# Optimization experiments

Hardware: AMD Instinct MI355X
Metric: run time of the kernel (lower is better)

## Reference

```python
import jax, jax.numpy as jnp
import numpy as np

D = 256; NH = 8; DH = D // NH; NL = 4; NP = 4; DFFN = 1024
SPATIAL = [(128, 128), (64, 64), (32, 32), (16, 16)]
LEN_IN = sum(h * w for h, w in SPATIAL)
N, LQ = 8, 1000


def _ln(x, g, b, eps=1e-5):
    m = jnp.mean(x, -1, keepdims=True)
    v = jnp.mean((x - m) ** 2, -1, keepdims=True)
    return (x - m) * jax.lax.rsqrt(v + eps) * g + b


def _ms_deform_core(value, loc, attn_w):
    # value (N,Len_in,NH,DH); loc (N,Lq,NH,NL,NP,2) in [0,1]; attn_w (N,Lq,NH,NL,NP)
    n, lq = loc.shape[0], loc.shape[1]
    out = jnp.zeros((n, NH, lq, DH), value.dtype)
    start = 0
    for l, (Hl, Wl) in enumerate(SPATIAL):
        v = value[:, start:start + Hl * Wl].transpose(0, 2, 1, 3)  # (N,NH,HW,DH)
        start += Hl * Wl
        # grid_sample-style mapping, align_corners=False, zero padding
        x = loc[:, :, :, l, :, 0] * Wl - 0.5  # (N,Lq,NH,NP)
        y = loc[:, :, :, l, :, 1] * Hl - 0.5
        x0 = jnp.floor(x); y0 = jnp.floor(y)
        lx = x - x0; ly = y - y0
        x0i = x0.astype(jnp.int32); y0i = y0.astype(jnp.int32)
        acc = jnp.zeros((n, NH, lq, NP, DH), value.dtype)
        for dy, dx, w in ((0, 0, (1 - ly) * (1 - lx)), (0, 1, (1 - ly) * lx),
                          (1, 0, ly * (1 - lx)), (1, 1, ly * lx)):
            xi = x0i + dx; yi = y0i + dy
            valid = ((xi >= 0) & (xi < Wl) & (yi >= 0) & (yi < Hl)).astype(value.dtype)
            idx = jnp.clip(yi, 0, Hl - 1) * Wl + jnp.clip(xi, 0, Wl - 1)  # (N,Lq,NH,NP)
            idx = idx.transpose(0, 2, 1, 3).reshape(n, NH, lq * NP)
            g = jnp.take_along_axis(v, idx[..., None], axis=2).reshape(n, NH, lq, NP, DH)
            acc = acc + g * (w * valid).transpose(0, 2, 1, 3)[..., None]
        out = out + jnp.sum(acc * attn_w[:, :, :, l].transpose(0, 2, 1, 3)[..., None], axis=3)
    return out.transpose(0, 2, 1, 3).reshape(n, lq, D)


def setup_inputs() -> dict:
    key = jax.random.key(0)
    ks = jax.random.split(key, 16)
    s = 0.02
    inp = {
        'tgt': jax.random.normal(ks[0], (N, LQ, D), jnp.float32),
        'query_pos': jax.random.normal(ks[1], (N, LQ, D), jnp.float32),
        'reference_points': jax.random.uniform(ks[2], (N, LQ, NL, 2), jnp.float32),
        'src': jax.random.normal(ks[3], (N, LEN_IN, D), jnp.float32),
        'spatial_shapes': jnp.array(SPATIAL, jnp.int32),
        'level_start_index': jnp.array(np.cumsum([0] + [h * w for h, w in SPATIAL[:-1]]), jnp.int32),
        # self-attention
        'sa_in_w': jax.random.normal(ks[4], (3 * D, D), jnp.float32) * s,
        'sa_in_b': jnp.zeros((3 * D,), jnp.float32),
        'sa_out_w': jax.random.normal(ks[5], (D, D), jnp.float32) * s,
        'sa_out_b': jnp.zeros((D,), jnp.float32),
        'norm2_g': jnp.ones((D,), jnp.float32), 'norm2_b': jnp.zeros((D,), jnp.float32),
        # MSDeformAttn
        'off_w': jax.random.normal(ks[6], (NH * NL * NP * 2, D), jnp.float32) * s,
        'off_b': jax.random.normal(ks[7], (NH * NL * NP * 2,), jnp.float32) * s,
        'aw_w': jax.random.normal(ks[8], (NH * NL * NP, D), jnp.float32) * s,
        'aw_b': jnp.zeros((NH * NL * NP,), jnp.float32),
        'val_w': jax.random.normal(ks[9], (D, D), jnp.float32) * s,
        'val_b': jnp.zeros((D,), jnp.float32),
        'outp_w': jax.random.normal(ks[10], (D, D), jnp.float32) * s,
        'outp_b': jnp.zeros((D,), jnp.float32),
        'norm1_g': jnp.ones((D,), jnp.float32), 'norm1_b': jnp.zeros((D,), jnp.float32),
        # FFN
        'ffn_w1': jax.random.normal(ks[11], (DFFN, D), jnp.float32) * s,
        'ffn_b1': jnp.zeros((DFFN,), jnp.float32),
        'ffn_w2': jax.random.normal(ks[12], (D, DFFN), jnp.float32) * s,
        'ffn_b2': jnp.zeros((D,), jnp.float32),
        'norm3_g': jnp.ones((D,), jnp.float32), 'norm3_b': jnp.zeros((D,), jnp.float32),
    }
    return inp


def reference(tgt, query_pos, reference_points, src, spatial_shapes, level_start_index,
              sa_in_w, sa_in_b, sa_out_w, sa_out_b, norm2_g, norm2_b,
              off_w, off_b, aw_w, aw_b, val_w, val_b, outp_w, outp_b, norm1_g, norm1_b,
              ffn_w1, ffn_b1, ffn_w2, ffn_b2, norm3_g, norm3_b):
    n, lq, _ = tgt.shape
    # ---- self-attention (q = k = tgt + pos, v = tgt), eval mode (dropout off)
    qk = tgt + query_pos
    wq, wk, wv = sa_in_w[:D], sa_in_w[D:2 * D], sa_in_w[2 * D:]
    bq, bk, bv = sa_in_b[:D], sa_in_b[D:2 * D], sa_in_b[2 * D:]
    q = (qk @ wq.T + bq).reshape(n, lq, NH, DH)
    k = (qk @ wk.T + bk).reshape(n, lq, NH, DH)
    v = (tgt @ wv.T + bv).reshape(n, lq, NH, DH)
    scores = jnp.einsum('bqhd,bkhd->bhqk', q, k) / np.sqrt(DH).astype(np.float32)
    attn = jax.nn.softmax(scores, axis=-1)
    sa = jnp.einsum('bhqk,bkhd->bqhd', attn, v).reshape(n, lq, D) @ sa_out_w.T + sa_out_b
    tgt = _ln(tgt + sa, norm2_g, norm2_b)
    # ---- multi-scale deformable cross-attention
    query = tgt + query_pos
    value = (src @ val_w.T + val_b).reshape(n, LEN_IN, NH, DH)
    offsets = (query @ off_w.T + off_b).reshape(n, lq, NH, NL, NP, 2)
    aw = (query @ aw_w.T + aw_b).reshape(n, lq, NH, NL * NP)
    aw = jax.nn.softmax(aw, axis=-1).reshape(n, lq, NH, NL, NP)
    # offset normalizer: (W_l, H_l)
    norm = jnp.stack([spatial_shapes[:, 1], spatial_shapes[:, 0]], -1).astype(tgt.dtype)
    loc = reference_points[:, :, None, :, None, :] + offsets / norm[None, None, None, :, None, :]
    ca = _ms_deform_core(value, loc, aw) @ outp_w.T + outp_b
    tgt = _ln(tgt + ca, norm1_g, norm1_b)
    # ---- FFN
    ff = jax.nn.relu(tgt @ ffn_w1.T + ffn_b1) @ ffn_w2.T + ffn_b2
    tgt = _ln(tgt + ff, norm3_g, norm3_b)
    return tgt
```

## Files before the change

### kernel.cpp

```cpp
#include <hip/hip_runtime.h>
#include <hip/hip_bf16.h>

#define D 256
#define NH 8
#define DH 32
#define NL 4
#define NP 4
#define DFFN 1024
#define LEN_IN 21760
#define NB 8
#define LQ 1000

typedef __hip_bfloat16 bf16;
typedef __attribute__((ext_vector_type(8))) short s8v;
typedef __attribute__((ext_vector_type(4))) float f4v;

template <typename T> __device__ inline T fromF(float x);
template <> __device__ inline float fromF<float>(float x) { return x; }
template <> __device__ inline bf16 fromF<bf16>(float x) { return __float2bfloat16(x); }

__device__ inline short bfr(float f) {
    unsigned u = __float_as_uint(f);
    u += 0x7fff + ((u >> 16) & 1);
    return (short)(u >> 16);
}
__device__ inline s8v pack8(float4 x, float4 y) {
    s8v r;
    r[0] = bfr(x.x); r[1] = bfr(x.y); r[2] = bfr(x.z); r[3] = bfr(x.w);
    r[4] = bfr(y.x); r[5] = bfr(y.y); r[6] = bfr(y.z); r[7] = bfr(y.w);
    return r;
}

__device__ inline unsigned cvtpk(float a, float b) {
    unsigned r;
    asm("v_cvt_pk_bf16_f32 %0, %1, %2" : "=v"(r) : "v"(a), "v"(b));
    return r;
}
__device__ inline s8v pkcvt8(float4 a, float4 b) {
    union { s8v v; unsigned u[4]; } r;
    r.u[0] = cvtpk(a.x, a.y);
    r.u[1] = cvtpk(a.z, a.w);
    r.u[2] = cvtpk(b.x, b.y);
    r.u[3] = cvtpk(b.z, b.w);
    return r.v;
}

__device__ __forceinline__ void gload_lds16(const void* gsrc, void* ldst) {
    __builtin_amdgcn_global_load_lds(
        (const __attribute__((address_space(1))) unsigned int*)gsrc,
        (__attribute__((address_space(3))) unsigned int*)ldst,
        16, 0, 0);
}

__global__ __launch_bounds__(256) void pack_weights(const float* __restrict__ s0, const float* __restrict__ s1,
                                                    const float* __restrict__ s2, const float* __restrict__ s3,
                                                    const float* __restrict__ s4, const float* __restrict__ s5,
                                                    const float* __restrict__ s6, const float* __restrict__ s7,
                                                    bf16* __restrict__ dst) {
    int g = blockIdx.x * 256 + threadIdx.x;
    const float* s; int base;
    if      (g <  49152) { s = s0; base = 0;      }
    else if (g <  65536) { s = s1; base = 49152;  }
    else if (g <  81920) { s = s2; base = 65536;  }
    else if (g <  90112) { s = s3; base = 81920;  }
    else if (g < 106496) { s = s4; base = 90112;  }
    else if (g < 122880) { s = s5; base = 106496; }
    else if (g < 188416) { s = s6; base = 122880; }
    else                 { s = s7; base = 188416; }
    float4 v = ((const float4*)s)[g - base];
    short4 o; o.x = bfr(v.x); o.y = bfr(v.y); o.z = bfr(v.z); o.w = bfr(v.w);
    ((short4*)dst)[g] = o;
}

template <typename TA, typename TC, int MT, bool ADD2, int KK>
__global__ __launch_bounds__(256) void gemm_direct(const TA* __restrict__ A, const float* __restrict__ A2,
                                                   const bf16* __restrict__ W, const float* __restrict__ bias,
                                                   TC* __restrict__ C, int N, int do_relu) {
    const int tid = threadIdx.x;
    const int lane = tid & 63, wave = tid >> 6;
    const int fr = lane & 15, fq = lane >> 4;
    const int n0 = blockIdx.x * 128;
    const int wrow = blockIdx.y * (MT * 32) + (wave >> 1) * (MT * 16);
    const int wn = n0 + (wave & 1) * 64;

    const TA* ap[MT];
    const float* a2p[MT];
#pragma unroll
    for (int i = 0; i < MT; ++i) {
        size_t r = (size_t)(wrow + i * 16 + fr);
        ap[i] = A + r * KK + fq * 8;
        if constexpr (ADD2) a2p[i] = A2 + r * KK + fq * 8;
    }
    const bf16* wp[4];
#pragma unroll
    for (int j = 0; j < 4; ++j) wp[j] = W + (size_t)(wn + j * 16 + fr) * KK + fq * 8;

    f4v acc[MT][4];
#pragma unroll
    for (int i = 0; i < MT; ++i)
#pragma unroll
        for (int j = 0; j < 4; ++j) acc[i][j] = (f4v){0.f, 0.f, 0.f, 0.f};

    auto step = [&](int k0) {
        s8v bfv[4];
#pragma unroll
        for (int j = 0; j < 4; ++j) bfv[j] = *(const s8v*)(wp[j] + k0);
        s8v af[MT];
#pragma unroll
        for (int i = 0; i < MT; ++i) {
            if constexpr (sizeof(TA) == 2) {
                af[i] = *(const s8v*)((const bf16*)ap[i] + k0);
            } else {
                float4 x0 = *(const float4*)((const float*)ap[i] + k0);
                float4 x1 = *(const float4*)((const float*)ap[i] + k0 + 4);
                if constexpr (ADD2) {
                    float4 y0 = *(const float4*)(a2p[i] + k0);
                    float4 y1 = *(const float4*)(a2p[i] + k0 + 4);
                    x0.x += y0.x; x0.y += y0.y; x0.z += y0.z; x0.w += y0.w;
                    x1.x += y1.x; x1.y += y1.y; x1.z += y1.z; x1.w += y1.w;
                }
                af[i] = pkcvt8(x0, x1);
            }
        }
#pragma unroll
        for (int i = 0; i < MT; ++i)
#pragma unroll
            for (int j = 0; j < 4; ++j)
                acc[i][j] = __builtin_amdgcn_mfma_f32_16x16x32_bf16(af[i], bfv[j], acc[i][j], 0, 0, 0);
    };

    if constexpr (KK <= 256) {
#pragma unroll
        for (int k0 = 0; k0 < KK; k0 += 32) step(k0);
    } else {
#pragma unroll 4
        for (int k0 = 0; k0 < KK; k0 += 32) step(k0);
    }

#pragma unroll
    for (int j = 0; j < 4; ++j) {
        const int col = wn + j * 16 + fr;
        const float bb = bias[col];
#pragma unroll
        for (int i = 0; i < MT; ++i) {
            const int rbase = wrow + i * 16 + fq * 4;
#pragma unroll
            for (int r = 0; r < 4; ++r) {
                float v = acc[i][j][r] + bb;
                if (do_relu) v = fmaxf(v, 0.f);
                C[(size_t)(rbase + r) * N + col] = fromF<TC>(v);
            }
        }
    }
}

__global__ __launch_bounds__(256) void gemm_val(const float* __restrict__ A, const bf16* __restrict__ W,
                                                const float* __restrict__ bias, bf16* __restrict__ C) {
    __shared__ float As[4096];
    const int tid = threadIdx.x;
    const int lane = tid & 63, wave = tid >> 6;
    const int fr = lane & 15, fq = lane >> 4;
    const int m0 = blockIdx.y * 128;
    const int wm = (wave >> 1) * 64;
    const int wn = blockIdx.x * 128 + (wave & 1) * 64;

    int srow[4], soff[4];
#pragma unroll
    for (int g = 0; g < 4; ++g) {
        int s = g * 4096 + tid * 16;
        int r = s >> 7;
        srow[g] = r;
        soff[g] = (s & 127) ^ ((r & 7) << 4);
    }
    int rb[4][2];
#pragma unroll
    for (int i = 0; i < 4; ++i) {
        int r2 = wm + i * 16 + fr;
        rb[i][0] = r2 * 128 + ((fq * 32) ^ ((r2 & 7) << 4));
        rb[i][1] = r2 * 128 + ((fq * 32 + 16) ^ ((r2 & 7) << 4));
    }
    const bf16* wp[4];
#pragma unroll
    for (int j = 0; j < 4; ++j) wp[j] = W + (size_t)(wn + j * 16 + fr) * 256 + fq * 8;

    f4v acc[4][4];
#pragma unroll
    for (int i = 0; i < 4; ++i)
#pragma unroll
        for (int j = 0; j < 4; ++j) acc[i][j] = (f4v){0.f, 0.f, 0.f, 0.f};

#pragma unroll
    for (int kk = 0; kk < 8; ++kk) {
        const int k0 = kk * 32;
        __syncthreads();
#pragma unroll
        for (int g = 0; g < 4; ++g) {
            const char* gsrc = (const char*)(A + (size_t)(m0 + srow[g]) * 256 + k0) + soff[g];
            gload_lds16(gsrc, (char*)As + g * 4096 + tid * 16);
        }
        __syncthreads();
        s8v bfv[4];
#pragma unroll
        for (int j = 0; j < 4; ++j) bfv[j] = *(const s8v*)(wp[j] + k0);
        s8v af[4];
#pragma unroll
        for (int i = 0; i < 4; ++i) {
            float4 x0 = *(const float4*)((const char*)As + rb[i][0]);
            float4 x1 = *(const float4*)((const char*)As + rb[i][1]);
            af[i] = pkcvt8(x0, x1);
        }
#pragma unroll
        for (int i = 0; i < 4; ++i)
#pragma unroll
            for (int j = 0; j < 4; ++j)
                acc[i][j] = __builtin_amdgcn_mfma_f32_16x16x32_bf16(af[i], bfv[j], acc[i][j], 0, 0, 0);
    }

#pragma unroll
    for (int j = 0; j < 4; ++j) {
        const int col = wn + j * 16 + fr;
        const float bb = bias[col];
#pragma unroll
        for (int i = 0; i < 4; ++i) {
            const int rbase = m0 + wm + i * 16 + fq * 4;
#pragma unroll
            for (int r = 0; r < 4; ++r) {
                float v = acc[i][j][r] + bb;
                C[(size_t)(rbase + r) * 256 + col] = fromF<bf16>(v);
            }
        }
    }
}

__global__ __launch_bounds__(256) void attn_mfma(const float* __restrict__ q, const float* __restrict__ k,
                                                 const float* __restrict__ v, float* __restrict__ out) {
    const int h = blockIdx.y, n = blockIdx.z;
    const int tid = threadIdx.x, wave = tid >> 6, lane = tid & 63;
    const int fr = lane & 15, fq = lane >> 4;
    __shared__ short Ks[32 * 40];
    __shared__ short Vt[32 * 40];
    __shared__ short Pl[4][16 * 40];
    const int q0 = blockIdx.x * 64 + wave * 16;

    s8v qfrag;
    {
        int qr = q0 + fr; if (qr >= LQ) qr = LQ - 1;
        const float* qp = q + ((size_t)(n * LQ + qr)) * D + h * DH + fq * 8;
        float4 t0 = *(const float4*)qp;
        float4 t1 = *(const float4*)(qp + 4);
        const float sc = 0.17677669529663687f;
        t0.x *= sc; t0.y *= sc; t0.z *= sc; t0.w *= sc;
        t1.x *= sc; t1.y *= sc; t1.z *= sc; t1.w *= sc;
        qfrag = pack8(t0, t1);
    }

    f4v O0 = {0.f, 0.f, 0.f, 0.f}, O1 = {0.f, 0.f, 0.f, 0.f};
    float mrow[4] = {-1e30f, -1e30f, -1e30f, -1e30f};
    float lrow[4] = {0.f, 0.f, 0.f, 0.f};

    for (int kt = 0; kt < LQ; kt += 32) {
        __syncthreads();
        {
            int key = tid >> 3, d4 = (tid & 7) * 4;
            int gk = kt + key; if (gk >= LQ) gk = LQ - 1;
            const float* kp = k + ((size_t)(n * LQ + gk)) * D + h * DH + d4;
            float4 t = *(const float4*)kp;
            short4 pk; pk.x = bfr(t.x); pk.y = bfr(t.y); pk.z = bfr(t.z); pk.w = bfr(t.w);
            *(short4*)&Ks[key * 40 + d4] = pk;
        }
        {
            int d = tid & 31, key0 = (tid >> 5) * 4;
            float vv[4];
#pragma unroll
            for (int i = 0; i < 4; ++i) {
                int gk = kt + key0 + i; if (gk >= LQ) gk = LQ - 1;
                vv[i] = v[((size_t)(n * LQ + gk)) * D + h * DH + d];
            }
            short4 pk; pk.x = bfr(vv[0]); pk.y = bfr(vv[1]); pk.z = bfr(vv[2]); pk.w = bfr(vv[3]);
            *(short4*)&Vt[d * 40 + key0] = pk;
        }
        __syncthreads();

        f4v s0 = {0.f, 0.f, 0.f, 0.f}, s1 = {0.f, 0.f, 0.f, 0.f};
        s8v kf0 = *(s8v*)&Ks[fr * 40 + fq * 8];
        s8v kf1 = *(s8v*)&Ks[(16 + fr) * 40 + fq * 8];
        s0 = __builtin_amdgcn_mfma_f32_16x16x32_bf16(qfrag, kf0, s0, 0, 0, 0);
        s1 = __builtin_amdgcn_mfma_f32_16x16x32_bf16(qfrag, kf1, s1, 0, 0, 0);
        const bool val0 = (kt + fr) < LQ, val1 = (kt + 16 + fr) < LQ;

        float p0[4], p1[4], alpha[4];
#pragma unroll
        for (int r = 0; r < 4; ++r) {
            float a = val0 ? s0[r] : -1e30f;
            float b = val1 ? s1[r] : -1e30f;
            float mx = fmaxf(a, b);
            mx = fmaxf(mx, __shfl_xor(mx, 1, 64));
            mx = fmaxf(mx, __shfl_xor(mx, 2, 64));
            mx = fmaxf(mx, __shfl_xor(mx, 4, 64));
            mx = fmaxf(mx, __shfl_xor(mx, 8, 64));
            float mnew = fmaxf(mrow[r], mx);
            float al = __expf(mrow[r] - mnew);
            float e0 = __expf(a - mnew);
            float e1 = __expf(b - mnew);
            float ps = e0 + e1;
            ps += __shfl_xor(ps, 1, 64);
            ps += __shfl_xor(ps, 2, 64);
            ps += __shfl_xor(ps, 4, 64);
            ps += __shfl_xor(ps, 8, 64);
            lrow[r] = lrow[r] * al + ps;
            mrow[r] = mnew;
            alpha[r] = al;
            p0[r] = e0; p1[r] = e1;
        }

        short* pw = Pl[wave];
#pragma unroll
        for (int r = 0; r < 4; ++r) {
            pw[(fq * 4 + r) * 40 + fr] = bfr(p0[r]);
            pw[(fq * 4 + r) * 40 + 16 + fr] = bfr(p1[r]);
        }
        __builtin_amdgcn_s_waitcnt(0);
        s8v pfrag = *(s8v*)&pw[fr * 40 + fq * 8];
        s8v vf0 = *(s8v*)&Vt[fr * 40 + fq * 8];
        s8v vf1 = *(s8v*)&Vt[(16 + fr) * 40 + fq * 8];
#pragma unroll
        for (int r = 0; r < 4; ++r) { O0[r] *= alpha[r]; O1[r] *= alpha[r]; }
        O0 = __builtin_amdgcn_mfma_f32_16x16x32_bf16(pfrag, vf0, O0, 0, 0, 0);
        O1 = __builtin_amdgcn_mfma_f32_16x16x32_bf16(pfrag, vf1, O1, 0, 0, 0);
    }

#pragma unroll
    for (int r = 0; r < 4; ++r) {
        int qrow = q0 + fq * 4 + r;
        if (qrow < LQ) {
            float inv = 1.0f / lrow[r];
            float* op = out + ((size_t)(n * LQ + qrow)) * D + h * DH;
            op[fr] = O0[r] * inv;
            op[16 + fr] = O1[r] * inv;
        }
    }
}

__global__ __launch_bounds__(256) void ln_res_kernel(const float* __restrict__ base, const float* __restrict__ delta,
                                                     const float* __restrict__ g, const float* __restrict__ b,
                                                     float* __restrict__ out) {
    __shared__ float scratch[8];
    const size_t row = blockIdx.x;
    const int d = threadIdx.x;
    float x = base[row * D + d] + delta[row * D + d];
    float s1 = x, s2 = x * x;
    for (int o = 32; o > 0; o >>= 1) {
        s1 += __shfl_down(s1, o, 64);
        s2 += __shfl_down(s2, o, 64);
    }
    const int w = threadIdx.x >> 6, lane = threadIdx.x & 63;
    if (lane == 0) { scratch[w] = s1; scratch[4 + w] = s2; }
    __syncthreads();
    s1 = scratch[0] + scratch[1] + scratch[2] + scratch[3];
    s2 = scratch[4] + scratch[5] + scratch[6] + scratch[7];
    float mean = s1 * (1.0f / 256.0f);
    float var = s2 * (1.0f / 256.0f) - mean * mean;
    float rstd = rsqrtf(var + 1e-5f);
    float y = (x - mean) * rstd * g[d] + b[d];
    out[row * D + d] = y;
}

__global__ __launch_bounds__(256) void aw_softmax_kernel(float* __restrict__ aw, int ngrp) {
    int t = blockIdx.x * 256 + threadIdx.x;
    if (t >= ngrp) return;
    float* p = aw + (size_t)t * 16;
    float m = p[0];
#pragma unroll
    for (int i = 1; i < 16; ++i) m = fmaxf(m, p[i]);
    float s = 0.f;
    float e[16];
#pragma unroll
    for (int i = 0; i < 16; ++i) { e[i] = __expf(p[i] - m); s += e[i]; }
    float inv = 1.0f / s;
#pragma unroll
    for (int i = 0; i < 16; ++i) p[i] = e[i] * inv;
}

__global__ __launch_bounds__(256) void deform_kernel(const bf16* __restrict__ value, const float* __restrict__ offs,
                                                     const float* __restrict__ aw, const float* __restrict__ refp,
                                                     float* __restrict__ out) {
    const int h = blockIdx.y, n = blockIdx.z;
    const int tid = threadIdx.x;
    const int wave = tid >> 6, lane = tid & 63;
    const int qi = blockIdx.x * 4 + wave;
    const int c = lane & 15;
    const int l = lane >> 4;
    const size_t row = (size_t)n * LQ + qi;
    const int W = 128 >> l, H = 128 >> l;
    const int START[4] = {0, 16384, 20480, 21504};
    const float invW = 1.0f / W, invH = 1.0f / H;

    const float rx = refp[(row * NL + l) * 2 + 0];
    const float ry = refp[(row * NL + l) * 2 + 1];
    const bf16* vbase = value + ((size_t)n * LEN_IN + START[l]) * D + h * DH + 2 * c;
    const float* offp = offs + row * D + (h * NL + l) * NP * 2;
    const float* awp = aw + row * 128 + h * 16 + l * 4;

    float acc0 = 0.f, acc1 = 0.f;
#pragma unroll
    for (int p = 0; p < 4; ++p) {
        float ox = offp[p * 2 + 0];
        float oy = offp[p * 2 + 1];
        float wa = awp[p];
        float x = (rx + ox * invW) * W - 0.5f;
        float y = (ry + oy * invH) * H - 0.5f;
        float xf = floorf(x), yf = floorf(y);
        float lx = x - xf, ly = y - yf;
        int x0 = (int)xf, y0 = (int)yf;
        int x1 = x0 + 1, y1 = y0 + 1;
        float vx0 = (x0 >= 0 && x0 < W) ? 1.f : 0.f;
        float vx1 = (x1 >= 0 && x1 < W) ? 1.f : 0.f;
        float vy0 = (y0 >= 0 && y0 < H) ? 1.f : 0.f;
        float vy1 = (y1 >= 0 && y1 < H) ? 1.f : 0.f;
        int x0c = min(max(x0, 0), W - 1), x1c = min(max(x1, 0), W - 1);
        int y0c = min(max(y0, 0), H - 1), y1c = min(max(y1, 0), H - 1);
        float w00 = wa * (1.f - ly) * (1.f - lx) * vy0 * vx0;
        float w01 = wa * (1.f - ly) * lx * vy0 * vx1;
        float w10 = wa * ly * (1.f - lx) * vy1 * vx0;
        float w11 = wa * ly * lx * vy1 * vx1;
        unsigned u00 = *(const unsigned*)(vbase + (size_t)(y0c * W + x0c) * D);
        unsigned u01 = *(const unsigned*)(vbase + (size_t)(y0c * W + x1c) * D);
        unsigned u10 = *(const unsigned*)(vbase + (size_t)(y1c * W + x0c) * D);
        unsigned u11 = *(const unsigned*)(vbase + (size_t)(y1c * W + x1c) * D);
        acc0 += w00 * __uint_as_float(u00 << 16) + w01 * __uint_as_float(u01 << 16)
              + w10 * __uint_as_float(u10 << 16) + w11 * __uint_as_float(u11 << 16);
        acc1 += w00 * __uint_as_float(u00 & 0xffff0000u) + w01 * __uint_as_float(u01 & 0xffff0000u)
              + w10 * __uint_as_float(u10 & 0xffff0000u) + w11 * __uint_as_float(u11 & 0xffff0000u);
    }
    acc0 += __shfl_xor(acc0, 16, 64); acc0 += __shfl_xor(acc0, 32, 64);
    acc1 += __shfl_xor(acc1, 16, 64); acc1 += __shfl_xor(acc1, 32, 64);
    if (l == 0) {
        float2 st = {acc0, acc1};
        *(float2*)(out + row * D + h * DH + 2 * c) = st;
    }
}

extern "C" void kernel_launch(void* const* d_in, const int* in_sizes, int n_in,
                              void* d_out, int out_size, void* d_ws, size_t ws_size,
                              hipStream_t stream) {
    const float* tgt = (const float*)d_in[0];
    const float* qpos = (const float*)d_in[1];
    const float* refp = (const float*)d_in[2];
    const float* src = (const float*)d_in[3];
    const float* sa_in_w = (const float*)d_in[6];
    const float* sa_in_b = (const float*)d_in[7];
    const float* sa_out_w = (const float*)d_in[8];
    const float* sa_out_b = (const float*)d_in[9];
    const float* norm2_g = (const float*)d_in[10];
    const float* norm2_b = (const float*)d_in[11];
    const float* off_w = (const float*)d_in[12];
    const float* off_b = (const float*)d_in[13];
    const float* aw_w = (const float*)d_in[14];
    const float* aw_b = (const float*)d_in[15];
    const float* val_w = (const float*)d_in[16];
    const float* val_b = (const float*)d_in[17];
    const float* outp_w = (const float*)d_in[18];
    const float* outp_b = (const float*)d_in[19];
    const float* norm1_g = (const float*)d_in[20];
    const float* norm1_b = (const float*)d_in[21];
    const float* ffn_w1 = (const float*)d_in[22];
    const float* ffn_b1 = (const float*)d_in[23];
    const float* ffn_w2 = (const float*)d_in[24];
    const float* ffn_b2 = (const float*)d_in[25];
    const float* norm3_g = (const float*)d_in[26];
    const float* norm3_b = (const float*)d_in[27];
    float* outp = (float*)d_out;

    const size_t NTOK = (size_t)NB * LQ;
    const size_t NE = NTOK * D;
    float* w = (float*)d_ws;
    size_t off = 0;
    auto alloc = [&](size_t n) { float* p = w + off; off += n; return p; };
    float* bufA = alloc(NE);
    float* bufB = alloc(NE);
    float* bufC = alloc(NE);
    float* bufD = alloc(NE);
    float* tgt2 = alloc(NE);
    float* tgt3 = alloc(NE);
    float* awb = alloc(NTOK * 128);
    bf16* mid = (bf16*)alloc(NTOK * DFFN / 2);
    bf16* value = (bf16*)alloc((size_t)NB * LEN_IN * D / 2);
    bf16* wb = (bf16*)alloc(507904);

    const bf16* wq    = wb;
    const bf16* wk    = wb + 65536;
    const bf16* wv    = wb + 131072;
    const bf16* wo    = wb + 196608;
    const bf16* woff  = wb + 262144;
    const bf16* waw   = wb + 327680;
    const bf16* wval  = wb + 360448;
    const bf16* woutp = wb + 425984;
    const bf16* wf1   = wb + 491520;
    const bf16* wf2   = wb + 753664;

    const int M8K = (int)NTOK;
    dim3 g8(2, M8K / 64);
    dim3 g8aw(1, M8K / 64);
    dim3 g8f1(DFFN / 128, M8K / 64);
    dim3 gVal(2, (NB * LEN_IN) / 128);

    pack_weights<<<992, 256, 0, stream>>>(sa_in_w, sa_out_w, off_w, aw_w, val_w, outp_w, ffn_w1, ffn_w2, wb);

    gemm_direct<float, float, 2, true, 256><<<g8, 256, 0, stream>>>(tgt, qpos, wq, sa_in_b, bufB, D, 0);
    gemm_direct<float, float, 2, true, 256><<<g8, 256, 0, stream>>>(tgt, qpos, wk, sa_in_b + 256, bufC, D, 0);
    gemm_direct<float, float, 2, false, 256><<<g8, 256, 0, stream>>>(tgt, nullptr, wv, sa_in_b + 512, bufD, D, 0);
    attn_mfma<<<dim3((LQ + 63) / 64, NH, NB), 256, 0, stream>>>(bufB, bufC, bufD, bufA);
    gemm_direct<float, float, 2, false, 256><<<g8, 256, 0, stream>>>(bufA, nullptr, wo, sa_out_b, bufB, D, 0);
    ln_res_kernel<<<NTOK, 256, 0, stream>>>(tgt, bufB, norm2_g, norm2_b, tgt2);

    gemm_val<<<gVal, 256, 0, stream>>>(src, wval, val_b, value);
    gemm_direct<float, float, 2, true, 256><<<g8, 256, 0, stream>>>(tgt2, qpos, woff, off_b, bufD, D, 0);
    gemm_direct<float, float, 2, true, 256><<<g8aw, 256, 0, stream>>>(tgt2, qpos, waw, aw_b, awb, 128, 0);
    aw_softmax_kernel<<<(int)(NTOK * NH + 255) / 256, 256, 0, stream>>>(awb, (int)(NTOK * NH));
    deform_kernel<<<dim3(LQ / 4, NH, NB), 256, 0, stream>>>(value, bufD, awb, refp, bufA);
    gemm_direct<float, float, 2, false, 256><<<g8, 256, 0, stream>>>(bufA, nullptr, woutp, outp_b, bufB, D, 0);
    ln_res_kernel<<<NTOK, 256, 0, stream>>>(tgt2, bufB, norm1_g, norm1_b, tgt3);

    gemm_direct<float, bf16, 2, false, 256><<<g8f1, 256, 0, stream>>>(tgt3, nullptr, wf1, ffn_b1, mid, DFFN, 1);
    gemm_direct<bf16, float, 2, false, 1024><<<g8, 256, 0, stream>>>(mid, nullptr, wf2, ffn_b2, bufC, D, 0);
    ln_res_kernel<<<NTOK, 256, 0, stream>>>(tgt3, bufC, norm3_g, norm3_b, outp);
}
```

Before: 652.1 us.

## Replace GEMMs with LDS-staged A-tile kernel and precompute query+pos sums

Adds a gemm_ldsA kernel that loads a whole R-row A tile (full K) into swizzled LDS once. Each of four waves then covers 64 output columns from that shared tile, replacing per-wave direct global A loads and the old gemm_val kernel. The tgt+query_pos add is computed once into a buffer by a new add_f4 kernel, so the Q, K, offset and attention-weight GEMMs no longer redo it. Tiles shrink to 16 or 32 rows, giving many more blocks. The costs are extra kernel launches and a temporary buffer, plus a large LDS footprint for the K=1024 FFN2 case that may limit occupancy.

```diff
diff --git a/kernel.cpp b/kernel.cpp
--- a/kernel.cpp
+++ b/kernel.cpp
@@ -72,6 +72,103 @@
     ((short4*)dst)[g] = o;
 }
 
+__global__ __launch_bounds__(256) void add_f4(const float4* __restrict__ a, const float4* __restrict__ b,
+                                              float4* __restrict__ o) {
+    int i = blockIdx.x * 256 + threadIdx.x;
+    float4 x = a[i], y = b[i];
+    x.x += y.x; x.y += y.y; x.z += y.z; x.w += y.w;
+    o[i] = x;
+}
+
+template <typename TA, typename TC, int R, int KK>
+__global__ __launch_bounds__(256) void gemm_ldsA(const TA* __restrict__ A, const bf16* __restrict__ W,
+                                                 const float* __restrict__ bias, TC* __restrict__ C,
+                                                 int N, int do_relu) {
+    constexpr int RB = KK * sizeof(TA);
+    constexpr int LDSB = R * RB;
+    constexpr int NSLOT = LDSB / 4096;
+    constexpr int MI = R / 16;
+    __shared__ char As[LDSB];
+
+    const int tid = threadIdx.x;
+    const int lane = tid & 63, wave = tid >> 6;
+    const int fr = lane & 15, fq = lane >> 4;
+    const int m0 = blockIdx.y * R;
+    const int wn = blockIdx.x * 256 + wave * 64;
+
+#pragma unroll
+    for (int i = 0; i < NSLOT; ++i) {
+        int s = i * 4096 + tid * 16;
+        int r = s / RB;
+        int c = (s % RB) ^ ((r & 7) << 4);
+        const char* gsrc = (const char*)A + (size_t)(m0 + r) * RB + c;
+        gload_lds16(gsrc, As + i * 4096 + tid * 16);
+    }
+
+    const bf16* wp[4];
+#pragma unroll
+    for (int j = 0; j < 4; ++j) wp[j] = W + (size_t)(wn + j * 16 + fr) * KK + fq * 8;
+
+    f4v acc[MI][4];
+#pragma unroll
+    for (int i = 0; i < MI; ++i)
+#pragma unroll
+        for (int j = 0; j < 4; ++j) acc[i][j] = (f4v){0.f, 0.f, 0.f, 0.f};
+
+    __syncthreads();
+
+    auto step = [&](int kk) {
+        s8v bfv[4];
+#pragma unroll
+        for (int j = 0; j < 4; ++j) bfv[j] = *(const s8v*)(wp[j] + kk * 32);
+        s8v af[MI];
+#pragma unroll
+        for (int i = 0; i < MI; ++i) {
+            const int row = i * 16 + fr;
+            const int sw = (fr & 7) << 4;
+            if constexpr (sizeof(TA) == 2) {
+                int c0 = (kk * 64 + fq * 16) ^ sw;
+                af[i] = *(const s8v*)(As + row * RB + c0);
+            } else {
+                int c0 = (kk * 128 + fq * 32) ^ sw;
+                int c1 = (kk * 128 + fq * 32 + 16) ^ sw;
+                float4 x0 = *(const float4*)(As + row * RB + c0);
+                float4 x1 = *(const float4*)(As + row * RB + c1);
+                af[i] = pkcvt8(x0, x1);
+            }
+        }
+#pragma unroll
+        for (int i = 0; i < MI; ++i)
+#pragma unroll
+            for (int j = 0; j < 4; ++j)
+                acc[i][j] = __builtin_amdgcn_mfma_f32_16x16x32_bf16(af[i], bfv[j], acc[i][j], 0, 0, 0);
+    };
+
+    if constexpr (KK <= 256) {
+#pragma unroll
+        for (int kk = 0; kk < KK / 32; ++kk) step(kk);
+    } else {
+#pragma unroll 4
+        for (int kk = 0; kk < KK / 32; ++kk) step(kk);
+    }
+
+#pragma unroll
+    for (int j = 0; j < 4; ++j) {
+        const int col = wn + j * 16 + fr;
+        const float bb = bias[col];
+#pragma unroll
+        for (int i = 0; i < MI; ++i) {
+            const int rbase = m0 + i * 16 + fq * 4;
+#pragma unroll
+            for (int r = 0; r < 4; ++r) {
+                float v = acc[i][j][r] + bb;
+                if (do_relu) v = fmaxf(v, 0.f);
+                C[(size_t)(rbase + r) * N + col] = fromF<TC>(v);
+            }
+        }
+    }
+}
+
 template <typename TA, typename TC, int MT, bool ADD2, int KK>
 __global__ __launch_bounds__(256) void gemm_direct(const TA* __restrict__ A, const float* __restrict__ A2,
                                                    const bf16* __restrict__ W, const float* __restrict__ bias,
@@ -129,13 +226,8 @@
                 acc[i][j] = __builtin_amdgcn_mfma_f32_16x16x32_bf16(af[i], bfv[j], acc[i][j], 0, 0, 0);
     };
 
-    if constexpr (KK <= 256) {
-#pragma unroll
-        for (int k0 = 0; k0 < KK; k0 += 32) step(k0);
-    } else {
-#pragma unroll 4
-        for (int k0 = 0; k0 < KK; k0 += 32) step(k0);
-    }
+#pragma unroll
+    for (int k0 = 0; k0 < KK; k0 += 32) step(k0);
 
 #pragma unroll
     for (int j = 0; j < 4; ++j) {
@@ -149,84 +241,6 @@
                 float v = acc[i][j][r] + bb;
                 if (do_relu) v = fmaxf(v, 0.f);
                 C[(size_t)(rbase + r) * N + col] = fromF<TC>(v);
-            }
-        }
-    }
-}
-
-__global__ __launch_bounds__(256) void gemm_val(const float* __restrict__ A, const bf16* __restrict__ W,
-                                                const float* __restrict__ bias, bf16* __restrict__ C) {
-    __shared__ float As[4096];
-    const int tid = threadIdx.x;
-    const int lane = tid & 63, wave = tid >> 6;
-    const int fr = lane & 15, fq = lane >> 4;
-    const int m0 = blockIdx.y * 128;
-    const int wm = (wave >> 1) * 64;
-    const int wn = blockIdx.x * 128 + (wave & 1) * 64;
-
-    int srow[4], soff[4];
-#pragma unroll
-    for (int g = 0; g < 4; ++g) {
-        int s = g * 4096 + tid * 16;
-        int r = s >> 7;
-        srow[g] = r;
-        soff[g] = (s & 127) ^ ((r & 7) << 4);
-    }
-    int rb[4][2];
-#pragma unroll
-    for (int i = 0; i < 4; ++i) {
-        int r2 = wm + i * 16 + fr;
-        rb[i][0] = r2 * 128 + ((fq * 32) ^ ((r2 & 7) << 4));
-        rb[i][1] = r2 * 128 + ((fq * 32 + 16) ^ ((r2 & 7) << 4));
-    }
-    const bf16* wp[4];
-#pragma unroll
-    for (int j = 0; j < 4; ++j) wp[j] = W + (size_t)(wn + j * 16 + fr) * 256 + fq * 8;
-
-    f4v acc[4][4];
-#pragma unroll
-    for (int i = 0; i < 4; ++i)
-#pragma unroll
-        for (int j = 0; j < 4; ++j) acc[i][j] = (f4v){0.f, 0.f, 0.f, 0.f};
-
-#pragma unroll
-    for (int kk = 0; kk < 8; ++kk) {
-        const int k0 = kk * 32;
-        __syncthreads();
-#pragma unroll
-        for (int g = 0; g < 4; ++g) {
-            const char* gsrc = (const char*)(A + (size_t)(m0 + srow[g]) * 256 + k0) + soff[g];
-            gload_lds16(gsrc, (char*)As + g * 4096 + tid * 16);
-        }
-        __syncthreads();
-        s8v bfv[4];
-#pragma unroll
-        for (int j = 0; j < 4; ++j) bfv[j] = *(const s8v*)(wp[j] + k0);
-        s8v af[4];
-#pragma unroll
-        for (int i = 0; i < 4; ++i) {
-            float4 x0 = *(const float4*)((const char*)As + rb[i][0]);
-            float4 x1 = *(const float4*)((const char*)As + rb[i][1]);
-            af[i] = pkcvt8(x0, x1);
-        }
-#pragma unroll
-        for (int i = 0; i < 4; ++i)
-#pragma unroll
-            for (int j = 0; j < 4; ++j)
-                acc[i][j] = __builtin_amdgcn_mfma_f32_16x16x32_bf16(af[i], bfv[j], acc[i][j], 0, 0, 0);
-    }
-
-#pragma unroll
-    for (int j = 0; j < 4; ++j) {
-        const int col = wn + j * 16 + fr;
-        const float bb = bias[col];
-#pragma unroll
-        for (int i = 0; i < 4; ++i) {
-            const int rbase = m0 + wm + i * 16 + fq * 4;
-#pragma unroll
-            for (int r = 0; r < 4; ++r) {
-                float v = acc[i][j][r] + bb;
-                C[(size_t)(rbase + r) * 256 + col] = fromF<bf16>(v);
             }
         }
     }
@@ -499,29 +513,31 @@
     const bf16* wf2   = wb + 753664;
 
     const int M8K = (int)NTOK;
-    dim3 g8(2, M8K / 64);
-    dim3 g8aw(1, M8K / 64);
-    dim3 g8f1(DFFN / 128, M8K / 64);
-    dim3 gVal(2, (NB * LEN_IN) / 128);
+    dim3 g16(1, M8K / 16);
+    dim3 gf1(DFFN / 256, M8K / 16);
+    dim3 gVal(1, (NB * LEN_IN) / 32);
+    dim3 gAw(1, M8K / 64);
 
     pack_weights<<<992, 256, 0, stream>>>(sa_in_w, sa_out_w, off_w, aw_w, val_w, outp_w, ffn_w1, ffn_w2, wb);
 
-    gemm_direct<float, float, 2, true, 256><<<g8, 256, 0, stream>>>(tgt, qpos, wq, sa_in_b, bufB, D, 0);
-    gemm_direct<float, float, 2, true, 256><<<g8, 256, 0, stream>>>(tgt, qpos, wk, sa_in_b + 256, bufC, D, 0);
-    gemm_direct<float, float, 2, false, 256><<<g8, 256, 0, stream>>>(tgt, nullptr, wv, sa_in_b + 512, bufD, D, 0);
+    add_f4<<<2000, 256, 0, stream>>>((const float4*)tgt, (const float4*)qpos, (float4*)bufA);
+    gemm_ldsA<float, float, 16, 256><<<g16, 256, 0, stream>>>(bufA, wq, sa_in_b, bufB, D, 0);
+    gemm_ldsA<float, float, 16, 256><<<g16, 256, 0, stream>>>(bufA, wk, sa_in_b + 256, bufC, D, 0);
+    gemm_ldsA<float, float, 16, 256><<<g16, 256, 0, stream>>>(tgt, wv, sa_in_b + 512, bufD, D, 0);
     attn_mfma<<<dim3((LQ + 63) / 64, NH, NB), 256, 0, stream>>>(bufB, bufC, bufD, bufA);
-    gemm_direct<float, float, 2, false, 256><<<g8, 256, 0, stream>>>(bufA, nullptr, wo, sa_out_b, bufB, D, 0);
+    gemm_ldsA<float, float, 16, 256><<<g16, 256, 0, stream>>>(bufA, wo, sa_out_b, bufB, D, 0);
     ln_res_kernel<<<NTOK, 256, 0, stream>>>(tgt, bufB, norm2_g, norm2_b, tgt2);
 
-    gemm_val<<<gVal, 256, 0, stream>>>(src, wval, val_b, value);
-    gemm_direct<float, float, 2, true, 256><<<g8, 256, 0, stream>>>(tgt2, qpos, woff, off_b, bufD, D, 0);
-    gemm_direct<float, float, 2, true, 256><<<g8aw, 256, 0, stream>>>(tgt2, qpos, waw, aw_b, awb, 128, 0);
+    gemm_ldsA<float, bf16, 32, 256><<<gVal, 256, 0, stream>>>(src, wval, val_b, value, D, 0);
+    add_f4<<<2000, 256, 0, stream>>>((const float4*)tgt2, (const float4*)qpos, (float4*)bufA);
+    gemm_ldsA<float, float, 16, 256><<<g16, 256, 0, stream>>>(bufA, woff, off_b, bufD, D, 0);
+    gemm_direct<float, float, 2, false, 256><<<gAw, 256, 0, stream>>>(bufA, nullptr, waw, aw_b, awb, 128, 0);
     aw_softmax_kernel<<<(int)(NTOK * NH + 255) / 256, 256, 0, stream>>>(awb, (int)(NTOK * NH));
     deform_kernel<<<dim3(LQ / 4, NH, NB), 256, 0, stream>>>(value, bufD, awb, refp, bufA);
-    gemm_direct<float, float, 2, false, 256><<<g8, 256, 0, stream>>>(bufA, nullptr, woutp, outp_b, bufB, D, 0);
+    gemm_ldsA<float, float, 16, 256><<<g16, 256, 0, stream>>>(bufA, woutp, outp_b, bufB, D, 0);
     ln_res_kernel<<<NTOK, 256, 0, stream>>>(tgt2, bufB, norm1_g, norm1_b, tgt3);
 
-    gemm_direct<float, bf16, 2, false, 256><<<g8f1, 256, 0, stream>>>(tgt3, nullptr, wf1, ffn_b1, mid, DFFN, 1);
-    gemm_direct<bf16, float, 2, false, 1024><<<g8, 256, 0, stream>>>(mid, nullptr, wf2, ffn_b2, bufC, D, 0);
+    gemm_ldsA<float, bf16, 16, 256><<<gf1, 256, 0, stream>>>(tgt3, wf1, ffn_b1, mid, DFFN, 1);
+    gemm_ldsA<bf16, float, 16, 1024><<<g16, 256, 0, stream>>>(mid, wf2, ffn_b2, bufC, D, 0);
     ln_res_kernel<<<NTOK, 256, 0, stream>>>(tgt3, bufC, norm3_g, norm3_b, outp);
 }
```

Result: slower. 687.1 us (+5.4%).
